# Kernel optimization log

Hardware: AMD Instinct MI355X
Metric: run time of the kernel (lower is better)

The kernel has to match this reference:

```python
import jax, jax.numpy as jnp
import numpy as np

NEG_SLOPE = 0.2  # PyG GATConv default leaky_relu slope


def _gat_layer(h, mask, W, att_src, att_dst, bias, concat):
    """PyG-style GATConv (eval mode, add_self_loops handled via mask diag).
    h: [B,N,D_in], mask: [B,N,N] bool (mask[b,i,j]=True if edge j->i, incl. self loop)
    W: [D_in, H*C], att_src/att_dst: [H,C], bias: [H*C] or [C].
    """
    B, N, _ = h.shape
    H, C = att_src.shape
    x = (h @ W).reshape(B, N, H, C)                       # [B,N,H,C]
    e_src = jnp.einsum('bnhc,hc->bnh', x, att_src)        # score contrib of source j
    e_dst = jnp.einsum('bnhc,hc->bnh', x, att_dst)        # score contrib of target i
    # scores[b,i,j,h] = leaky_relu(e_dst_i + e_src_j)
    s = jax.nn.leaky_relu(e_dst[:, :, None, :] + e_src[:, None, :, :], NEG_SLOPE)
    s = jnp.where(mask[..., None], s, -jnp.inf)
    alpha = jax.nn.softmax(s, axis=2)                     # softmax over neighbors j
    out = jnp.einsum('bijh,bjhc->bihc', alpha, x)         # aggregate
    out = out.reshape(B, N, H * C) if concat else out.mean(axis=2)
    return out + bias


def setup_inputs() -> dict:
    key = jax.random.key(0)
    ks = jax.random.split(key, 16)
    B, T, N, F_in = 4, 8, 2000, 158
    D, H = 128, 4
    C = D // H  # 32
    x_alpha = jax.random.normal(ks[0], (B, T, N, F_in), dtype=jnp.float32)
    sector_graph = (jax.random.uniform(ks[1], (B, N, N)) > 0.98).astype(jnp.float32)
    g = lambda k, shp, fan: jax.random.normal(k, shp, dtype=jnp.float32) / np.sqrt(fan)
    return {
        'x_alpha': x_alpha,
        'sector_graph': sector_graph,
        'W_in': g(ks[2], (F_in, D), F_in), 'b_in': jnp.zeros((D,), jnp.float32),
        'ln_g': jnp.ones((D,), jnp.float32), 'ln_b': jnp.zeros((D,), jnp.float32),
        'W0': g(ks[3], (D, H * C), D), 'as0': g(ks[4], (H, C), C), 'ad0': g(ks[5], (H, C), C),
        'bias0': jnp.zeros((H * C,), jnp.float32),
        'W1': g(ks[6], (D, H * C), D), 'as1': g(ks[7], (H, C), C), 'ad1': g(ks[8], (H, C), C),
        'bias1': jnp.zeros((C,), jnp.float32),
        'W_out': g(ks[9], (C, D), C), 'b_out': jnp.zeros((D,), jnp.float32),
    }


def reference(x_alpha, sector_graph, W_in, b_in, ln_g, ln_b,
              W0, as0, ad0, bias0, W1, as1, ad1, bias1, W_out, b_out):
    B, T, N, _ = x_alpha.shape
    x = x_alpha[:, -1]                                    # [B,N,F]
    # input_proj: Linear -> LayerNorm -> ReLU (dropout is identity in eval)
    h = x @ W_in + b_in
    mu = h.mean(-1, keepdims=True)
    var = ((h - mu) ** 2).mean(-1, keepdims=True)
    h = (h - mu) / jnp.sqrt(var + 1e-5) * ln_g + ln_b
    h = jax.nn.relu(h)                                    # [B,N,128]
    # edge mask with self loops (PyG add_self_loops=True)
    eye = jnp.eye(N, dtype=bool)
    mask = (sector_graph > 0) | eye[None]
    # layer 0: concat=True, out dim 128 == in dim -> residual, elu (not last layer)
    h0 = _gat_layer(h, mask, W0, as0, ad0, bias0, concat=True)
    h = h + jax.nn.elu(h0)
    # layer 1 (last): concat=False, out dim 32 != 128 -> no residual, no elu
    h = _gat_layer(h, mask, W1, as1, ad1, bias1, concat=False)  # [B,N,32]
    return h @ W_out + b_out                              # [B,N,128]
```

## Files before the change

### kernel.cpp

```cpp
#include <hip/hip_runtime.h>

typedef unsigned short u16;

__device__ __forceinline__ float us2f(u16 u){
  unsigned int x = ((unsigned int)u) << 16;
  return __uint_as_float(x);
}
__device__ __forceinline__ u16 f2us(float f){
  unsigned int u = __float_as_uint(f);
  unsigned int r = (u + 0x7fffu + ((u >> 16) & 1u)) >> 16;
  return (u16)r;
}
__device__ __forceinline__ float wredSum(float v){
  #pragma unroll
  for (int o = 32; o > 0; o >>= 1) v += __shfl_xor(v, o, 64);
  return v;
}
__device__ __forceinline__ float g32Sum(float v){
  #pragma unroll
  for (int o = 16; o > 0; o >>= 1) v += __shfl_xor(v, o, 32);
  return v;
}
__device__ __forceinline__ float g8Sum(float v){
  #pragma unroll
  for (int o = 4; o > 0; o >>= 1) v += __shfl_xor(v, o, 32);
  return v;
}

#define ACAP 128
#define RB 16

__global__ __launch_bounds__(256) void k_inln_gat0(
    const float* __restrict__ xA, const float* __restrict__ Win,
    const float* __restrict__ bin, const float* __restrict__ lng,
    const float* __restrict__ lnb, const float* __restrict__ W0,
    const float* __restrict__ as0, const float* __restrict__ ad0,
    float* __restrict__ h, u16* __restrict__ x0,
    float* __restrict__ es, float* __restrict__ ed)
{
  __shared__ float xs[RB][160];
  __shared__ float Wt[2][8][128];
  const int t = threadIdx.x;
  const int row0 = blockIdx.x * RB;
  const int tx = t & 31, ty = t >> 5;
  const int c0 = tx * 4, rbase = ty * 2;
  const int wk = ty;
  const int b = row0 / 2000;
  const int n0 = row0 - b * 2000;
  const size_t xbase = (((size_t)b * 8 + 7) * 2000 + n0) * 158;

  for (int idx = t; idx < RB * 160; idx += 256){
    int r = idx / 160, k = idx - r * 160;
    xs[r][k] = (k < 158) ? xA[xbase + (size_t)r * 158 + k] : 0.f;
  }
  *(float4*)&Wt[0][wk][c0] = *(const float4*)&Win[(size_t)wk * 128 + c0];
  __syncthreads();

  float acc[2][4];
  #pragma unroll
  for (int r = 0; r < 2; r++)
    #pragma unroll
    for (int c = 0; c < 4; c++) acc[r][c] = 0.f;

  const int NT1 = 20;
  for (int tl = 0; tl < NT1; tl++){
    const int cur = tl & 1;
    float4 wreg = make_float4(0.f, 0.f, 0.f, 0.f);
    const bool hn = (tl + 1 < NT1);
    if (hn){
      int k = (tl + 1) * 8 + wk;
      if (k < 158) wreg = *(const float4*)&Win[(size_t)k * 128 + c0];
    }
    const int k0 = tl * 8;
    #pragma unroll
    for (int kh = 0; kh < 2; kh++){
      float4 a[2];
      #pragma unroll
      for (int r = 0; r < 2; r++) a[r] = *(const float4*)&xs[rbase + r][k0 + kh * 4];
      #pragma unroll
      for (int kk = 0; kk < 4; kk++){
        float4 w = *(const float4*)&Wt[cur][kh * 4 + kk][c0];
        #pragma unroll
        for (int r = 0; r < 2; r++){
          float av = ((const float*)&a[r])[kk];
          acc[r][0] = fmaf(av, w.x, acc[r][0]);
          acc[r][1] = fmaf(av, w.y, acc[r][1]);
          acc[r][2] = fmaf(av, w.z, acc[r][2]);
          acc[r][3] = fmaf(av, w.w, acc[r][3]);
        }
      }
    }
    if (hn) *(float4*)&Wt[cur ^ 1][wk][c0] = wreg;
    __syncthreads();
  }

  {
    float4 bi = *(const float4*)&bin[c0];
    float4 g  = *(const float4*)&lng[c0];
    float4 be = *(const float4*)&lnb[c0];
    #pragma unroll
    for (int r = 0; r < 2; r++){
      float a0 = acc[r][0] + bi.x, a1 = acc[r][1] + bi.y;
      float a2 = acc[r][2] + bi.z, a3 = acc[r][3] + bi.w;
      float s  = g32Sum(a0 + a1 + a2 + a3);
      float sq = g32Sum(a0*a0 + a1*a1 + a2*a2 + a3*a3);
      float mu  = s * (1.f / 128.f);
      float var = sq * (1.f / 128.f) - mu * mu;
      float inv = rsqrtf(var + 1e-5f);
      float v0 = fmaxf((a0 - mu) * inv * g.x + be.x, 0.f);
      float v1 = fmaxf((a1 - mu) * inv * g.y + be.y, 0.f);
      float v2 = fmaxf((a2 - mu) * inv * g.z + be.z, 0.f);
      float v3 = fmaxf((a3 - mu) * inv * g.w + be.w, 0.f);
      *(float4*)&xs[rbase + r][c0] = make_float4(v0, v1, v2, v3);
      *(float4*)&h[(size_t)(row0 + rbase + r) * 128 + c0] = make_float4(v0, v1, v2, v3);
    }
  }
  *(float4*)&Wt[0][wk][c0] = *(const float4*)&W0[(size_t)wk * 128 + c0];
  __syncthreads();

  #pragma unroll
  for (int r = 0; r < 2; r++)
    #pragma unroll
    for (int c = 0; c < 4; c++) acc[r][c] = 0.f;
  const int NT2 = 16;
  for (int tl = 0; tl < NT2; tl++){
    const int cur = tl & 1;
    float4 wreg = make_float4(0.f, 0.f, 0.f, 0.f);
    const bool hn = (tl + 1 < NT2);
    if (hn) wreg = *(const float4*)&W0[(size_t)((tl + 1) * 8 + wk) * 128 + c0];
    const int k0 = tl * 8;
    #pragma unroll
    for (int kh = 0; kh < 2; kh++){
      float4 a[2];
      #pragma unroll
      for (int r = 0; r < 2; r++) a[r] = *(const float4*)&xs[rbase + r][k0 + kh * 4];
      #pragma unroll
      for (int kk = 0; kk < 4; kk++){
        float4 w = *(const float4*)&Wt[cur][kh * 4 + kk][c0];
        #pragma unroll
        for (int r = 0; r < 2; r++){
          float av = ((const float*)&a[r])[kk];
          acc[r][0] = fmaf(av, w.x, acc[r][0]);
          acc[r][1] = fmaf(av, w.y, acc[r][1]);
          acc[r][2] = fmaf(av, w.z, acc[r][2]);
          acc[r][3] = fmaf(av, w.w, acc[r][3]);
        }
      }
    }
    if (hn) *(float4*)&Wt[cur ^ 1][wk][c0] = wreg;
    __syncthreads();
  }

  {
    float4 av = *(const float4*)&as0[c0];
    float4 dv = *(const float4*)&ad0[c0];
    const int hh = tx >> 3;
    #pragma unroll
    for (int r = 0; r < 2; r++){
      ushort4 o;
      o.x = f2us(acc[r][0]); o.y = f2us(acc[r][1]);
      o.z = f2us(acc[r][2]); o.w = f2us(acc[r][3]);
      *(ushort4*)(x0 + (size_t)(row0 + rbase + r) * 128 + c0) = o;
      float ps = acc[r][0]*av.x + acc[r][1]*av.y + acc[r][2]*av.z + acc[r][3]*av.w;
      float pd = acc[r][0]*dv.x + acc[r][1]*dv.y + acc[r][2]*dv.z + acc[r][3]*dv.w;
      ps = g8Sum(ps); pd = g8Sum(pd);
      if ((tx & 7) == 0){
        es[(size_t)(row0 + rbase + r) * 4 + hh] = ps;
        ed[(size_t)(row0 + rbase + r) * 4 + hh] = pd;
      }
    }
  }
}

__global__ __launch_bounds__(256) void k_gat_pre(
    const float* __restrict__ hin, const float* __restrict__ W,
    const float* __restrict__ asv, const float* __restrict__ adv,
    u16* __restrict__ x0, float* __restrict__ es, float* __restrict__ ed)
{
  __shared__ float xs[RB][128];
  __shared__ float Wt[2][8][128];
  const int t = threadIdx.x;
  const int row0 = blockIdx.x * RB;
  const int tx = t & 31, ty = t >> 5;
  const int c0 = tx * 4, rbase = ty * 2;
  const int wk = ty;

  for (int f = t; f < RB * 32; f += 256){
    int r = f >> 5, cq = (f & 31) * 4;
    *(float4*)&xs[r][cq] = *(const float4*)&hin[(size_t)(row0 + r) * 128 + cq];
  }
  *(float4*)&Wt[0][wk][c0] = *(const float4*)&W[(size_t)wk * 128 + c0];
  __syncthreads();

  float acc[2][4];
  #pragma unroll
  for (int r = 0; r < 2; r++)
    #pragma unroll
    for (int c = 0; c < 4; c++) acc[r][c] = 0.f;

  const int NT = 16;
  for (int tl = 0; tl < NT; tl++){
    const int cur = tl & 1;
    float4 wreg = make_float4(0.f, 0.f, 0.f, 0.f);
    const bool hn = (tl + 1 < NT);
    if (hn) wreg = *(const float4*)&W[(size_t)((tl + 1) * 8 + wk) * 128 + c0];
    const int k0 = tl * 8;
    #pragma unroll
    for (int kh = 0; kh < 2; kh++){
      float4 a[2];
      #pragma unroll
      for (int r = 0; r < 2; r++) a[r] = *(const float4*)&xs[rbase + r][k0 + kh * 4];
      #pragma unroll
      for (int kk = 0; kk < 4; kk++){
        float4 w = *(const float4*)&Wt[cur][kh * 4 + kk][c0];
        #pragma unroll
        for (int r = 0; r < 2; r++){
          float av = ((const float*)&a[r])[kk];
          acc[r][0] = fmaf(av, w.x, acc[r][0]);
          acc[r][1] = fmaf(av, w.y, acc[r][1]);
          acc[r][2] = fmaf(av, w.z, acc[r][2]);
          acc[r][3] = fmaf(av, w.w, acc[r][3]);
        }
      }
    }
    if (hn) *(float4*)&Wt[cur ^ 1][wk][c0] = wreg;
    __syncthreads();
  }

  {
    float4 av = *(const float4*)&asv[c0];
    float4 dv = *(const float4*)&adv[c0];
    const int hh = tx >> 3;
    #pragma unroll
    for (int r = 0; r < 2; r++){
      ushort4 o;
      o.x = f2us(acc[r][0]); o.y = f2us(acc[r][1]);
      o.z = f2us(acc[r][2]); o.w = f2us(acc[r][3]);
      *(ushort4*)(x0 + (size_t)(row0 + rbase + r) * 128 + c0) = o;
      float ps = acc[r][0]*av.x + acc[r][1]*av.y + acc[r][2]*av.z + acc[r][3]*av.w;
      float pd = acc[r][0]*dv.x + acc[r][1]*dv.y + acc[r][2]*dv.z + acc[r][3]*dv.w;
      ps = g8Sum(ps); pd = g8Sum(pd);
      if ((tx & 7) == 0){
        es[(size_t)(row0 + rbase + r) * 4 + hh] = ps;
        ed[(size_t)(row0 + rbase + r) * 4 + hh] = pd;
      }
    }
  }
}

template<int LAYER>
__global__ __launch_bounds__(256) void k_attn(
    const float* __restrict__ sg,
    u16* __restrict__ adj, int* __restrict__ cnt,
    const u16* __restrict__ x0,
    const float* __restrict__ es, const float* __restrict__ ed,
    const float* __restrict__ bias, float* __restrict__ hio,
    const float* __restrict__ Wout, const float* __restrict__ bout,
    float* __restrict__ outv)
{
  __shared__ int   idx_s[4][ACAP];
  __shared__ float sc[4][4][132];
  __shared__ int   cnt_s[4];
  const int t = threadIdx.x;
  const int w = t >> 6;
  const int l = t & 63;
  const int bi = blockIdx.x * 4 + w;
  const int b = bi / 2000;
  const int i = bi - b * 2000;

  if (LAYER == 0){
    if (l == 0) cnt_s[w] = 0;
    const float4* row4 = (const float4*)(sg + (size_t)bi * 2000);
    #pragma unroll
    for (int q = 0; q < 8; q++){
      int f4 = q * 64 + l;
      if (f4 < 500){
        float4 v = row4[f4];
        int j0 = f4 * 4;
        #pragma unroll
        for (int u = 0; u < 4; u++){
          int j = j0 + u;
          float vv = (&v.x)[u];
          if (vv > 0.f || j == i){
            int p = atomicAdd(&cnt_s[w], 1);
            if (p < ACAP){
              idx_s[w][p] = j;
              adj[(size_t)bi * ACAP + p] = (u16)j;
            }
          }
        }
      }
    }
    if (l == 0) cnt[bi] = min(cnt_s[w], ACAP);
  } else {
    int mg = cnt[bi];
    if (l == 0) cnt_s[w] = mg;
    if (l < mg)      idx_s[w][l]      = (int)adj[(size_t)bi * ACAP + l];
    if (64 + l < mg) idx_s[w][64 + l] = (int)adj[(size_t)bi * ACAP + 64 + l];
  }
  __syncthreads();
  const int m = min(cnt_s[w], ACAP);

  float4 edv = *(const float4*)&ed[(size_t)bi * 4];
  float q0 = 0.f, q1 = 0.f, q2 = 0.f, q3 = 0.f;
  #pragma unroll
  for (int rep = 0; rep < 2; rep++){
    int e = rep * 64 + l;
    if (e < m){
      int j = idx_s[w][e];
      float4 esv = *(const float4*)&es[((size_t)b * 2000 + j) * 4];
      float s0 = edv.x + esv.x; s0 = s0 > 0.f ? s0 : 0.2f * s0;
      float s1 = edv.y + esv.y; s1 = s1 > 0.f ? s1 : 0.2f * s1;
      float s2 = edv.z + esv.z; s2 = s2 > 0.f ? s2 : 0.2f * s2;
      float s3 = edv.w + esv.w; s3 = s3 > 0.f ? s3 : 0.2f * s3;
      float p0 = __expf(s0), p1 = __expf(s1), p2 = __expf(s2), p3 = __expf(s3);
      sc[w][0][e] = p0; sc[w][1][e] = p1; sc[w][2][e] = p2; sc[w][3][e] = p3;
      q0 += p0; q1 += p1; q2 += p2; q3 += p3;
    }
  }
  q0 = wredSum(q0); q1 = wredSum(q1); q2 = wredSum(q2); q3 = wredSum(q3);
  __syncthreads();

  const int hh = l >> 4;
  float qh = hh < 2 ? (hh == 0 ? q0 : q1) : (hh == 2 ? q2 : q3);
  float inv = 1.f / qh;
  float a0 = 0.f, a1 = 0.f;
  const u16* x0b = x0 + (size_t)b * 2000 * 128 + 2 * l;
  #pragma unroll 8
  for (int e = 0; e < m; e++){
    float p = sc[w][hh][e];
    int j = idx_s[w][e];
    unsigned int pk = *(const unsigned int*)(x0b + (size_t)j * 128);
    a0 = fmaf(p, us2f((u16)(pk & 0xffffu)), a0);
    a1 = fmaf(p, us2f((u16)(pk >> 16)), a1);
  }
  a0 *= inv; a1 *= inv;

  if (LAYER == 0){
    float2 bb = *(const float2*)&bias[2 * l];
    float v0 = a0 + bb.x; v0 = v0 > 0.f ? v0 : (__expf(v0) - 1.f);
    float v1 = a1 + bb.y; v1 = v1 > 0.f ? v1 : (__expf(v1) - 1.f);
    float2* hp = (float2*)&hio[(size_t)bi * 128 + 2 * l];
    float2 ho = *hp;
    *hp = make_float2(ho.x + v0, ho.y + v1);
  } else {
    float s0 = a0 + __shfl_xor(a0, 16); s0 += __shfl_xor(s0, 32);
    float s1 = a1 + __shfl_xor(a1, 16); s1 += __shfl_xor(s1, 32);
    float mv0 = s0 * 0.25f, mv1 = s1 * 0.25f;
    if (l < 16){
      float2 bb = *(const float2*)&bias[2 * l];
      mv0 += bb.x; mv1 += bb.y;
    }
    float2 bo = *(const float2*)&bout[2 * l];
    float o0 = bo.x, o1 = bo.y;
    #pragma unroll
    for (int p = 0; p < 16; p++){
      float mk0 = __shfl(mv0, p);
      float mk1 = __shfl(mv1, p);
      float2 w0 = *(const float2*)&Wout[(size_t)(2 * p) * 128 + 2 * l];
      float2 w1 = *(const float2*)&Wout[(size_t)(2 * p + 1) * 128 + 2 * l];
      o0 = fmaf(mk0, w0.x, o0); o1 = fmaf(mk0, w0.y, o1);
      o0 = fmaf(mk1, w1.x, o0); o1 = fmaf(mk1, w1.y, o1);
    }
    *(float2*)&outv[(size_t)bi * 128 + 2 * l] = make_float2(o0, o1);
  }
}

extern "C" void kernel_launch(void* const* d_in, const int* in_sizes, int n_in,
                              void* d_out, int out_size, void* d_ws, size_t ws_size,
                              hipStream_t stream) {
  const float* xA   = (const float*)d_in[0];
  const float* sg   = (const float*)d_in[1];
  const float* Win  = (const float*)d_in[2];
  const float* bin  = (const float*)d_in[3];
  const float* lng  = (const float*)d_in[4];
  const float* lnb  = (const float*)d_in[5];
  const float* W0   = (const float*)d_in[6];
  const float* as0  = (const float*)d_in[7];
  const float* ad0  = (const float*)d_in[8];
  const float* b0   = (const float*)d_in[9];
  const float* W1   = (const float*)d_in[10];
  const float* as1  = (const float*)d_in[11];
  const float* ad1  = (const float*)d_in[12];
  const float* b1   = (const float*)d_in[13];
  const float* Wout = (const float*)d_in[14];
  const float* bout = (const float*)d_in[15];

  char* ws = (char*)d_ws;
  float* h    = (float*)(ws);
  u16*   x0   = (u16*)  (ws + 4096000);
  float* es   = (float*)(ws + 6144000);
  float* ed   = (float*)(ws + 6272000);
  u16*   adj  = (u16*)  (ws + 6400000);
  int*   cnt  = (int*)  (ws + 8448000);

  k_inln_gat0 <<<500, 256, 0, stream>>>(xA, Win, bin, lng, lnb, W0, as0, ad0, h, x0, es, ed);
  k_attn<0>   <<<2000, 256, 0, stream>>>(sg, adj, cnt, x0, es, ed, b0, h, nullptr, nullptr, nullptr);
  k_gat_pre   <<<500, 256, 0, stream>>>(h, W1, as1, ad1, x0, es, ed);
  k_attn<1>   <<<2000, 256, 0, stream>>>(nullptr, adj, cnt, x0, es, ed, b1, nullptr, Wout, bout, (float*)d_out);
}
```

Baseline: 200.5 us.

## Fuse layer-1 projection into layer-0 attention and use ballot-based neighbor compaction

Removes the separate k_gat_pre launch by computing the layer-1 linear projection, bf16 packing and attention logits inside the layer-0 attention kernel. Each block converts W1 to bf16 in shared memory and each wave does a per-row matvec with shuffles. Neighbor list building switches from shared atomics to wave ballot and popcount compaction, which also keeps neighbors in sorted order. The first kernel doubles rows per block to 32, halving its grid. The cost is that every one of 2000 blocks reloads and converts the full W1 into 32KB of LDS, and W1 is now rounded to bf16.

```diff
diff --git a/kernel.cpp b/kernel.cpp
--- a/kernel.cpp
+++ b/kernel.cpp
@@ -28,7 +28,7 @@
 }
 
 #define ACAP 128
-#define RB 16
+#define RBG 32
 
 __global__ __launch_bounds__(256) void k_inln_gat0(
     const float* __restrict__ xA, const float* __restrict__ Win,
@@ -38,27 +38,26 @@
     float* __restrict__ h, u16* __restrict__ x0,
     float* __restrict__ es, float* __restrict__ ed)
 {
-  __shared__ float xs[RB][160];
+  __shared__ float xs[RBG][160];
   __shared__ float Wt[2][8][128];
   const int t = threadIdx.x;
-  const int row0 = blockIdx.x * RB;
+  const int row0 = blockIdx.x * RBG;
   const int tx = t & 31, ty = t >> 5;
-  const int c0 = tx * 4, rbase = ty * 2;
+  const int c0 = tx * 4, rbase = ty * 4;
   const int wk = ty;
-  const int b = row0 / 2000;
-  const int n0 = row0 - b * 2000;
-  const size_t xbase = (((size_t)b * 8 + 7) * 2000 + n0) * 158;
-
-  for (int idx = t; idx < RB * 160; idx += 256){
+
+  for (int idx = t; idx < RBG * 160; idx += 256){
     int r = idx / 160, k = idx - r * 160;
-    xs[r][k] = (k < 158) ? xA[xbase + (size_t)r * 158 + k] : 0.f;
+    int row = row0 + r;
+    int b = row / 2000, n = row - b * 2000;
+    xs[r][k] = (k < 158) ? xA[(((size_t)b * 8 + 7) * 2000 + n) * 158 + k] : 0.f;
   }
   *(float4*)&Wt[0][wk][c0] = *(const float4*)&Win[(size_t)wk * 128 + c0];
   __syncthreads();
 
-  float acc[2][4];
-  #pragma unroll
-  for (int r = 0; r < 2; r++)
+  float acc[4][4];
+  #pragma unroll
+  for (int r = 0; r < 4; r++)
     #pragma unroll
     for (int c = 0; c < 4; c++) acc[r][c] = 0.f;
 
@@ -74,14 +73,14 @@
     const int k0 = tl * 8;
     #pragma unroll
     for (int kh = 0; kh < 2; kh++){
-      float4 a[2];
+      float4 a[4];
       #pragma unroll
-      for (int r = 0; r < 2; r++) a[r] = *(const float4*)&xs[rbase + r][k0 + kh * 4];
+      for (int r = 0; r < 4; r++) a[r] = *(const float4*)&xs[rbase + r][k0 + kh * 4];
       #pragma unroll
       for (int kk = 0; kk < 4; kk++){
         float4 w = *(const float4*)&Wt[cur][kh * 4 + kk][c0];
         #pragma unroll
-        for (int r = 0; r < 2; r++){
+        for (int r = 0; r < 4; r++){
           float av = ((const float*)&a[r])[kk];
           acc[r][0] = fmaf(av, w.x, acc[r][0]);
           acc[r][1] = fmaf(av, w.y, acc[r][1]);
@@ -99,7 +98,7 @@
     float4 g  = *(const float4*)&lng[c0];
     float4 be = *(const float4*)&lnb[c0];
     #pragma unroll
-    for (int r = 0; r < 2; r++){
+    for (int r = 0; r < 4; r++){
       float a0 = acc[r][0] + bi.x, a1 = acc[r][1] + bi.y;
       float a2 = acc[r][2] + bi.z, a3 = acc[r][3] + bi.w;
       float s  = g32Sum(a0 + a1 + a2 + a3);
@@ -119,7 +118,7 @@
   __syncthreads();
 
   #pragma unroll
-  for (int r = 0; r < 2; r++)
+  for (int r = 0; r < 4; r++)
     #pragma unroll
     for (int c = 0; c < 4; c++) acc[r][c] = 0.f;
   const int NT2 = 16;
@@ -131,14 +130,14 @@
     const int k0 = tl * 8;
     #pragma unroll
     for (int kh = 0; kh < 2; kh++){
-      float4 a[2];
+      float4 a[4];
       #pragma unroll
-      for (int r = 0; r < 2; r++) a[r] = *(const float4*)&xs[rbase + r][k0 + kh * 4];
+      for (int r = 0; r < 4; r++) a[r] = *(const float4*)&xs[rbase + r][k0 + kh * 4];
       #pragma unroll
       for (int kk = 0; kk < 4; kk++){
         float4 w = *(const float4*)&Wt[cur][kh * 4 + kk][c0];
         #pragma unroll
-        for (int r = 0; r < 2; r++){
+        for (int r = 0; r < 4; r++){
           float av = ((const float*)&a[r])[kk];
           acc[r][0] = fmaf(av, w.x, acc[r][0]);
           acc[r][1] = fmaf(av, w.y, acc[r][1]);
@@ -156,7 +155,7 @@
     float4 dv = *(const float4*)&ad0[c0];
     const int hh = tx >> 3;
     #pragma unroll
-    for (int r = 0; r < 2; r++){
+    for (int r = 0; r < 4; r++){
       ushort4 o;
       o.x = f2us(acc[r][0]); o.y = f2us(acc[r][1]);
       o.z = f2us(acc[r][2]); o.w = f2us(acc[r][3]);
@@ -172,134 +171,56 @@
   }
 }
 
-__global__ __launch_bounds__(256) void k_gat_pre(
-    const float* __restrict__ hin, const float* __restrict__ W,
-    const float* __restrict__ asv, const float* __restrict__ adv,
-    u16* __restrict__ x0, float* __restrict__ es, float* __restrict__ ed)
-{
-  __shared__ float xs[RB][128];
-  __shared__ float Wt[2][8][128];
-  const int t = threadIdx.x;
-  const int row0 = blockIdx.x * RB;
-  const int tx = t & 31, ty = t >> 5;
-  const int c0 = tx * 4, rbase = ty * 2;
-  const int wk = ty;
-
-  for (int f = t; f < RB * 32; f += 256){
-    int r = f >> 5, cq = (f & 31) * 4;
-    *(float4*)&xs[r][cq] = *(const float4*)&hin[(size_t)(row0 + r) * 128 + cq];
-  }
-  *(float4*)&Wt[0][wk][c0] = *(const float4*)&W[(size_t)wk * 128 + c0];
-  __syncthreads();
-
-  float acc[2][4];
-  #pragma unroll
-  for (int r = 0; r < 2; r++)
-    #pragma unroll
-    for (int c = 0; c < 4; c++) acc[r][c] = 0.f;
-
-  const int NT = 16;
-  for (int tl = 0; tl < NT; tl++){
-    const int cur = tl & 1;
-    float4 wreg = make_float4(0.f, 0.f, 0.f, 0.f);
-    const bool hn = (tl + 1 < NT);
-    if (hn) wreg = *(const float4*)&W[(size_t)((tl + 1) * 8 + wk) * 128 + c0];
-    const int k0 = tl * 8;
-    #pragma unroll
-    for (int kh = 0; kh < 2; kh++){
-      float4 a[2];
-      #pragma unroll
-      for (int r = 0; r < 2; r++) a[r] = *(const float4*)&xs[rbase + r][k0 + kh * 4];
-      #pragma unroll
-      for (int kk = 0; kk < 4; kk++){
-        float4 w = *(const float4*)&Wt[cur][kh * 4 + kk][c0];
-        #pragma unroll
-        for (int r = 0; r < 2; r++){
-          float av = ((const float*)&a[r])[kk];
-          acc[r][0] = fmaf(av, w.x, acc[r][0]);
-          acc[r][1] = fmaf(av, w.y, acc[r][1]);
-          acc[r][2] = fmaf(av, w.z, acc[r][2]);
-          acc[r][3] = fmaf(av, w.w, acc[r][3]);
-        }
-      }
-    }
-    if (hn) *(float4*)&Wt[cur ^ 1][wk][c0] = wreg;
-    __syncthreads();
-  }
-
-  {
-    float4 av = *(const float4*)&asv[c0];
-    float4 dv = *(const float4*)&adv[c0];
-    const int hh = tx >> 3;
-    #pragma unroll
-    for (int r = 0; r < 2; r++){
-      ushort4 o;
-      o.x = f2us(acc[r][0]); o.y = f2us(acc[r][1]);
-      o.z = f2us(acc[r][2]); o.w = f2us(acc[r][3]);
-      *(ushort4*)(x0 + (size_t)(row0 + rbase + r) * 128 + c0) = o;
-      float ps = acc[r][0]*av.x + acc[r][1]*av.y + acc[r][2]*av.z + acc[r][3]*av.w;
-      float pd = acc[r][0]*dv.x + acc[r][1]*dv.y + acc[r][2]*dv.z + acc[r][3]*dv.w;
-      ps = g8Sum(ps); pd = g8Sum(pd);
-      if ((tx & 7) == 0){
-        es[(size_t)(row0 + rbase + r) * 4 + hh] = ps;
-        ed[(size_t)(row0 + rbase + r) * 4 + hh] = pd;
-      }
-    }
-  }
-}
-
-template<int LAYER>
-__global__ __launch_bounds__(256) void k_attn(
-    const float* __restrict__ sg,
+__global__ __launch_bounds__(256) void k_attn0(
+    const float* __restrict__ sg, const float* __restrict__ hin,
     u16* __restrict__ adj, int* __restrict__ cnt,
     const u16* __restrict__ x0,
     const float* __restrict__ es, const float* __restrict__ ed,
-    const float* __restrict__ bias, float* __restrict__ hio,
-    const float* __restrict__ Wout, const float* __restrict__ bout,
-    float* __restrict__ outv)
+    const float* __restrict__ b0,
+    const float* __restrict__ W1, const float* __restrict__ as1,
+    const float* __restrict__ ad1,
+    u16* __restrict__ x1, float* __restrict__ es1, float* __restrict__ ed1)
 {
+  __shared__ u16   W1s[128][128];
   __shared__ int   idx_s[4][ACAP];
   __shared__ float sc[4][4][132];
-  __shared__ int   cnt_s[4];
   const int t = threadIdx.x;
-  const int w = t >> 6;
-  const int l = t & 63;
+  const int w = t >> 6, l = t & 63;
   const int bi = blockIdx.x * 4 + w;
   const int b = bi / 2000;
   const int i = bi - b * 2000;
 
-  if (LAYER == 0){
-    if (l == 0) cnt_s[w] = 0;
-    const float4* row4 = (const float4*)(sg + (size_t)bi * 2000);
-    #pragma unroll
-    for (int q = 0; q < 8; q++){
-      int f4 = q * 64 + l;
-      if (f4 < 500){
-        float4 v = row4[f4];
-        int j0 = f4 * 4;
-        #pragma unroll
-        for (int u = 0; u < 4; u++){
-          int j = j0 + u;
-          float vv = (&v.x)[u];
-          if (vv > 0.f || j == i){
-            int p = atomicAdd(&cnt_s[w], 1);
-            if (p < ACAP){
-              idx_s[w][p] = j;
-              adj[(size_t)bi * ACAP + p] = (u16)j;
-            }
-          }
+  for (int f = t; f < 4096; f += 256){
+    float4 v = *(const float4*)&W1[(size_t)f * 4];
+    int k = f >> 5, c = (f & 31) * 4;
+    ushort4 o; o.x = f2us(v.x); o.y = f2us(v.y); o.z = f2us(v.z); o.w = f2us(v.w);
+    *(ushort4*)&W1s[k][c] = o;
+  }
+
+  int cloc = 0;
+  const float4* row4 = (const float4*)(sg + (size_t)bi * 2000);
+  for (int q = 0; q < 8; q++){
+    int f4 = q * 64 + l;
+    float4 v = make_float4(0.f, 0.f, 0.f, 0.f);
+    if (f4 < 500) v = row4[f4];
+    #pragma unroll
+    for (int u = 0; u < 4; u++){
+      int j = f4 * 4 + u;
+      bool hit = (f4 < 500) && (((&v.x)[u] > 0.f) || (j == i));
+      unsigned long long mask = __ballot(hit);
+      if (hit){
+        int pos = cloc + (int)__popcll(mask & ((1ull << l) - 1ull));
+        if (pos < ACAP){
+          idx_s[w][pos] = j;
+          adj[(size_t)bi * ACAP + pos] = (u16)j;
         }
       }
-    }
-    if (l == 0) cnt[bi] = min(cnt_s[w], ACAP);
-  } else {
-    int mg = cnt[bi];
-    if (l == 0) cnt_s[w] = mg;
-    if (l < mg)      idx_s[w][l]      = (int)adj[(size_t)bi * ACAP + l];
-    if (64 + l < mg) idx_s[w][64 + l] = (int)adj[(size_t)bi * ACAP + 64 + l];
-  }
-  __syncthreads();
-  const int m = min(cnt_s[w], ACAP);
+      cloc += (int)__popcll(mask);
+    }
+  }
+  if (l == 0) cnt[bi] = min(cloc, ACAP);
+  const int m = min(cloc, ACAP);
+  __syncthreads();
 
   float4 edv = *(const float4*)&ed[(size_t)bi * 4];
   float q0 = 0.f, q1 = 0.f, q2 = 0.f, q3 = 0.f;
@@ -336,34 +257,116 @@
   }
   a0 *= inv; a1 *= inv;
 
-  if (LAYER == 0){
-    float2 bb = *(const float2*)&bias[2 * l];
-    float v0 = a0 + bb.x; v0 = v0 > 0.f ? v0 : (__expf(v0) - 1.f);
-    float v1 = a1 + bb.y; v1 = v1 > 0.f ? v1 : (__expf(v1) - 1.f);
-    float2* hp = (float2*)&hio[(size_t)bi * 128 + 2 * l];
-    float2 ho = *hp;
-    *hp = make_float2(ho.x + v0, ho.y + v1);
-  } else {
-    float s0 = a0 + __shfl_xor(a0, 16); s0 += __shfl_xor(s0, 32);
-    float s1 = a1 + __shfl_xor(a1, 16); s1 += __shfl_xor(s1, 32);
-    float mv0 = s0 * 0.25f, mv1 = s1 * 0.25f;
-    if (l < 16){
-      float2 bb = *(const float2*)&bias[2 * l];
-      mv0 += bb.x; mv1 += bb.y;
-    }
-    float2 bo = *(const float2*)&bout[2 * l];
-    float o0 = bo.x, o1 = bo.y;
-    #pragma unroll
-    for (int p = 0; p < 16; p++){
-      float mk0 = __shfl(mv0, p);
-      float mk1 = __shfl(mv1, p);
-      float2 w0 = *(const float2*)&Wout[(size_t)(2 * p) * 128 + 2 * l];
-      float2 w1 = *(const float2*)&Wout[(size_t)(2 * p + 1) * 128 + 2 * l];
-      o0 = fmaf(mk0, w0.x, o0); o1 = fmaf(mk0, w0.y, o1);
-      o0 = fmaf(mk1, w1.x, o0); o1 = fmaf(mk1, w1.y, o1);
-    }
-    *(float2*)&outv[(size_t)bi * 128 + 2 * l] = make_float2(o0, o1);
-  }
+  float2 hb = *(const float2*)&hin[(size_t)bi * 128 + 2 * l];
+  float2 bb = *(const float2*)&b0[2 * l];
+  float v0 = a0 + bb.x; v0 = v0 > 0.f ? v0 : (__expf(v0) - 1.f); v0 += hb.x;
+  float v1 = a1 + bb.y; v1 = v1 > 0.f ? v1 : (__expf(v1) - 1.f); v1 += hb.y;
+
+  float acc0 = 0.f, acc1 = 0.f;
+  #pragma unroll 16
+  for (int kp = 0; kp < 64; kp++){
+    float m0 = __shfl(v0, kp);
+    float m1 = __shfl(v1, kp);
+    unsigned int w0 = *(const unsigned int*)&W1s[2 * kp][2 * l];
+    unsigned int w1 = *(const unsigned int*)&W1s[2 * kp + 1][2 * l];
+    acc0 = fmaf(m0, us2f((u16)(w0 & 0xffffu)), acc0);
+    acc1 = fmaf(m0, us2f((u16)(w0 >> 16)), acc1);
+    acc0 = fmaf(m1, us2f((u16)(w1 & 0xffffu)), acc0);
+    acc1 = fmaf(m1, us2f((u16)(w1 >> 16)), acc1);
+  }
+  {
+    unsigned int pk = ((unsigned int)f2us(acc1) << 16) | (unsigned int)f2us(acc0);
+    *(unsigned int*)&x1[(size_t)bi * 128 + 2 * l] = pk;
+  }
+  {
+    float2 av = *(const float2*)&as1[2 * l];
+    float2 dv = *(const float2*)&ad1[2 * l];
+    float ps = acc0 * av.x + acc1 * av.y;
+    float pd = acc0 * dv.x + acc1 * dv.y;
+    #pragma unroll
+    for (int o = 1; o < 16; o <<= 1){ ps += __shfl_xor(ps, o); pd += __shfl_xor(pd, o); }
+    if ((l & 15) == 0){
+      es1[(size_t)bi * 4 + hh] = ps;
+      ed1[(size_t)bi * 4 + hh] = pd;
+    }
+  }
+}
+
+__global__ __launch_bounds__(256) void k_attn1(
+    const u16* __restrict__ adj, const int* __restrict__ cnt,
+    const u16* __restrict__ x1,
+    const float* __restrict__ es, const float* __restrict__ ed,
+    const float* __restrict__ b1,
+    const float* __restrict__ Wout, const float* __restrict__ bout,
+    float* __restrict__ outv)
+{
+  __shared__ int   idx_s[4][ACAP];
+  __shared__ float sc[4][4][132];
+  const int t = threadIdx.x;
+  const int w = t >> 6, l = t & 63;
+  const int bi = blockIdx.x * 4 + w;
+  const int b = bi / 2000;
+
+  const int mg = cnt[bi];
+  const int m = min(mg, ACAP);
+  if (l < m)      idx_s[w][l]      = (int)adj[(size_t)bi * ACAP + l];
+  if (64 + l < m) idx_s[w][64 + l] = (int)adj[(size_t)bi * ACAP + 64 + l];
+  __syncthreads();
+
+  float4 edv = *(const float4*)&ed[(size_t)bi * 4];
+  float q0 = 0.f, q1 = 0.f, q2 = 0.f, q3 = 0.f;
+  #pragma unroll
+  for (int rep = 0; rep < 2; rep++){
+    int e = rep * 64 + l;
+    if (e < m){
+      int j = idx_s[w][e];
+      float4 esv = *(const float4*)&es[((size_t)b * 2000 + j) * 4];
+      float s0 = edv.x + esv.x; s0 = s0 > 0.f ? s0 : 0.2f * s0;
+      float s1 = edv.y + esv.y; s1 = s1 > 0.f ? s1 : 0.2f * s1;
+      float s2 = edv.z + esv.z; s2 = s2 > 0.f ? s2 : 0.2f * s2;
+      float s3 = edv.w + esv.w; s3 = s3 > 0.f ? s3 : 0.2f * s3;
+      float p0 = __expf(s0), p1 = __expf(s1), p2 = __expf(s2), p3 = __expf(s3);
+      sc[w][0][e] = p0; sc[w][1][e] = p1; sc[w][2][e] = p2; sc[w][3][e] = p3;
+      q0 += p0; q1 += p1; q2 += p2; q3 += p3;
+    }
+  }
+  q0 = wredSum(q0); q1 = wredSum(q1); q2 = wredSum(q2); q3 = wredSum(q3);
+  __syncthreads();
+
+  const int hh = l >> 4;
+  float qh = hh < 2 ? (hh == 0 ? q0 : q1) : (hh == 2 ? q2 : q3);
+  float inv = 1.f / qh;
+  float a0 = 0.f, a1 = 0.f;
+  const u16* x1b = x1 + (size_t)b * 2000 * 128 + 2 * l;
+  #pragma unroll 8
+  for (int e = 0; e < m; e++){
+    float p = sc[w][hh][e];
+    int j = idx_s[w][e];
+    unsigned int pk = *(const unsigned int*)(x1b + (size_t)j * 128);
+    a0 = fmaf(p, us2f((u16)(pk & 0xffffu)), a0);
+    a1 = fmaf(p, us2f((u16)(pk >> 16)), a1);
+  }
+  a0 *= inv; a1 *= inv;
+
+  float s0 = a0 + __shfl_xor(a0, 16); s0 += __shfl_xor(s0, 32);
+  float s1 = a1 + __shfl_xor(a1, 16); s1 += __shfl_xor(s1, 32);
+  float mv0 = s0 * 0.25f, mv1 = s1 * 0.25f;
+  if (l < 16){
+    float2 bb = *(const float2*)&b1[2 * l];
+    mv0 += bb.x; mv1 += bb.y;
+  }
+  float2 bo = *(const float2*)&bout[2 * l];
+  float o0 = bo.x, o1 = bo.y;
+  #pragma unroll
+  for (int p = 0; p < 16; p++){
+    float mk0 = __shfl(mv0, p);
+    float mk1 = __shfl(mv1, p);
+    float2 w0 = *(const float2*)&Wout[(size_t)(2 * p) * 128 + 2 * l];
+    float2 w1 = *(const float2*)&Wout[(size_t)(2 * p + 1) * 128 + 2 * l];
+    o0 = fmaf(mk0, w0.x, o0); o1 = fmaf(mk0, w0.y, o1);
+    o0 = fmaf(mk1, w1.x, o0); o1 = fmaf(mk1, w1.y, o1);
+  }
+  *(float2*)&outv[(size_t)bi * 128 + 2 * l] = make_float2(o0, o1);
 }
 
 extern "C" void kernel_launch(void* const* d_in, const int* in_sizes, int n_in,
@@ -388,14 +391,17 @@
 
   char* ws = (char*)d_ws;
   float* h    = (float*)(ws);
-  u16*   x0   = (u16*)  (ws + 4096000);
-  float* es   = (float*)(ws + 6144000);
-  float* ed   = (float*)(ws + 6272000);
-  u16*   adj  = (u16*)  (ws + 6400000);
-  int*   cnt  = (int*)  (ws + 8448000);
-
-  k_inln_gat0 <<<500, 256, 0, stream>>>(xA, Win, bin, lng, lnb, W0, as0, ad0, h, x0, es, ed);
-  k_attn<0>   <<<2000, 256, 0, stream>>>(sg, adj, cnt, x0, es, ed, b0, h, nullptr, nullptr, nullptr);
-  k_gat_pre   <<<500, 256, 0, stream>>>(h, W1, as1, ad1, x0, es, ed);
-  k_attn<1>   <<<2000, 256, 0, stream>>>(nullptr, adj, cnt, x0, es, ed, b1, nullptr, Wout, bout, (float*)d_out);
-}
+  u16*   x0   = (u16*)  (ws +  4096000);
+  float* es0  = (float*)(ws +  6144000);
+  float* ed0  = (float*)(ws +  6272000);
+  u16*   adj  = (u16*)  (ws +  6400000);
+  int*   cnt  = (int*)  (ws +  8448000);
+  u16*   x1   = (u16*)  (ws +  8480000);
+  float* es1  = (float*)(ws + 10528000);
+  float* ed1  = (float*)(ws + 10656000);
+
+  k_inln_gat0 <<<250, 256, 0, stream>>>(xA, Win, bin, lng, lnb, W0, as0, ad0, h, x0, es0, ed0);
+  k_attn0     <<<2000, 256, 0, stream>>>(sg, h, adj, cnt, x0, es0, ed0, b0,
+                                         W1, as1, ad1, x1, es1, ed1);
+  k_attn1     <<<2000, 256, 0, stream>>>(adj, cnt, x1, es1, ed1, b1, Wout, bout, (float*)d_out);
+}
```

After: 227.4 us. 13.4% more time.
